# Optimization experiments

Hardware: AMD Instinct MI355X
Metric: run time of the kernel (lower is better)

Reference implementation:

```python
import jax, jax.numpy as jnp
import numpy as np

N_EMBD = 768
N_HEAD = 12


def setup_inputs() -> dict:
    key = jax.random.key(0)
    ks = jax.random.split(key, 5)
    B, T, C = 8, 1024, N_EMBD
    s_in = 1.0 / np.sqrt(C)
    x = jax.random.normal(ks[0], (B, T, C), dtype=jnp.float32)
    w_attn = jax.random.normal(ks[1], (C, 3 * C), dtype=jnp.float32) * s_in
    b_attn = jnp.zeros((3 * C,), dtype=jnp.float32)
    w_proj = jax.random.normal(ks[2], (C, C), dtype=jnp.float32) * s_in
    b_proj = jnp.zeros((C,), dtype=jnp.float32)
    return {"x": x, "w_attn": w_attn, "b_attn": b_attn,
            "w_proj": w_proj, "b_proj": b_proj}


def reference(x, w_attn, b_attn, w_proj, b_proj):
    B, T, C = x.shape
    H, hs = N_HEAD, C // N_HEAD
    qkv = x @ w_attn + b_attn                      # [B,T,3C]
    q, k, v = jnp.split(qkv, 3, axis=-1)
    # [B,H,T,hs]
    q = q.reshape(B, T, H, hs).transpose(0, 2, 1, 3)
    k = k.reshape(B, T, H, hs).transpose(0, 2, 1, 3)
    v = v.reshape(B, T, H, hs).transpose(0, 2, 1, 3)
    att = jnp.einsum('bhqd,bhkd->bhqk', q, k) * (1.0 / np.sqrt(hs))
    causal = jnp.tril(jnp.ones((T, T), dtype=bool))
    att = jnp.where(causal, att, -jnp.inf)
    att = jax.nn.softmax(att, axis=-1)
    y = jnp.einsum('bhqk,bhkd->bhqd', att, v)      # [B,H,T,hs]
    y = y.transpose(0, 2, 1, 3).reshape(B, T, C)
    return y @ w_proj + b_proj
```

## Files before the change

kernel.cpp:

```cpp
#include <hip/hip_runtime.h>
#include <hip/hip_bf16.h>
#include <stdint.h>

typedef unsigned short u16;
typedef short short8 __attribute__((ext_vector_type(8)));
typedef short short4v __attribute__((ext_vector_type(4)));
typedef float floatx4 __attribute__((ext_vector_type(4)));

__device__ __forceinline__ float b2f(u16 v) {
  union { unsigned int u; float f; } c; c.u = ((unsigned int)v) << 16; return c.f;
}
__device__ __forceinline__ u16 f2b(float f) {
  union { float f; unsigned int u; } c; c.f = f;
  unsigned int u = c.u;
  return (u16)((u + 0x7fffu + ((u >> 16) & 1u)) >> 16);
}

__device__ __forceinline__ void gld_lds16(const u16* g, u16* l) {
  __builtin_amdgcn_global_load_lds(
      (const __attribute__((address_space(1))) unsigned int*)g,
      (__attribute__((address_space(3))) unsigned int*)l,
      16, 0, 0);
}

__device__ __forceinline__ void tile_transpose_f2b(
    const float* __restrict__ in, u16* __restrict__ out,
    int inRS, int outRS, int rb, int cb, int tid)
{
  __shared__ __align__(16) u16 t[64][72];
  const int r = tid >> 2, sg = tid & 3;
  const float* ip = in + (long)(rb + r) * inRS + cb + sg * 16;
#pragma unroll
  for (int i = 0; i < 16; i += 4) {
    float4 f = *(const float4*)(ip + i);
    t[r][sg * 16 + i]     = f2b(f.x);
    t[r][sg * 16 + i + 1] = f2b(f.y);
    t[r][sg * 16 + i + 2] = f2b(f.z);
    t[r][sg * 16 + i + 3] = f2b(f.w);
  }
  __syncthreads();
  short8 v0, v1;
#pragma unroll
  for (int i = 0; i < 8; i++) v0[i] = (short)t[sg * 16 + i][r];
#pragma unroll
  for (int i = 0; i < 8; i++) v1[i] = (short)t[sg * 16 + 8 + i][r];
  *(short8*)(out + (long)(cb + r) * outRS + rb + sg * 16)     = v0;
  *(short8*)(out + (long)(cb + r) * outRS + rb + sg * 16 + 8) = v1;
}

__global__ __launch_bounds__(256) void prep(
    const float* __restrict__ x, u16* __restrict__ xb,
    const float* __restrict__ w_attn, u16* __restrict__ wTa,
    const float* __restrict__ w_proj, u16* __restrict__ wTp)
{
  const int bid = blockIdx.x, tid = threadIdx.x;
  if (bid < 6144) {
    int i = (bid * 256 + tid) * 4;
    float4 f = *(const float4*)(x + i);
    short4v v;
    v[0] = (short)f2b(f.x); v[1] = (short)f2b(f.y);
    v[2] = (short)f2b(f.z); v[3] = (short)f2b(f.w);
    *(short4v*)(xb + i) = v;
  } else if (bid < 6576) {
    int t = bid - 6144;
    tile_transpose_f2b(w_attn, wTa, 2304, 768, (t / 36) * 64, (t % 36) * 64, tid);
  } else {
    int t = bid - 6576;
    tile_transpose_f2b(w_proj, wTp, 768, 768, (t / 12) * 64, (t % 12) * 64, tid);
  }
}

__device__ __forceinline__ void store_out(u16* p, float v)  { *p = f2b(v); }
__device__ __forceinline__ void store_out(float* p, float v) { *p = v; }

template <int BM>
__device__ __forceinline__ void stage(
    const u16* __restrict__ A, const u16* __restrict__ Bt,
    long rowbase, long colbase, int K, int k0,
    u16* dA, u16* dB, int tid)
{
  const int c0 = tid, c1 = tid + 256;
  const int ar0 = c0 >> 2, ak0 = (c0 & 3) * 8;
  const int ar1 = c1 >> 2, ak1 = (c1 & 3) * 8;
  gld_lds16(A + (rowbase + ar0) * K + k0 + ak0, dA + c0 * 8);
  if (BM == 128)
    gld_lds16(A + (rowbase + ar1) * K + k0 + ak1, dA + c1 * 8);
  gld_lds16(Bt + (colbase + ar0) * K + k0 + ak0, dB + c0 * 8);
  gld_lds16(Bt + (colbase + ar1) * K + k0 + ak1, dB + c1 * 8);
}

template <typename OT, int BM, bool SPLIT>
__global__ __launch_bounds__(256) void gemm_bt_bias(
    const u16* __restrict__ A, const u16* __restrict__ Bt,
    const float* __restrict__ bias, OT* __restrict__ C, u16* __restrict__ vT,
    int M, int N, int K, int strideC)
{
  constexpr int WNF = (BM == 128) ? 4 : 2;
  __shared__ __align__(16) u16 sA[2][BM * 32];
  __shared__ __align__(16) u16 sB[2][128 * 32];
  const int tid = threadIdx.x;
  const int lane = tid & 63;
  const int wave = tid >> 6;
  const int wm = (BM == 128) ? (wave >> 1) * 64 : 0;
  const int wn = (BM == 128) ? (wave & 1) * 64 : wave * 32;
  const int l15 = lane & 15;
  const int q = lane >> 4;
  const long rowbase = (long)blockIdx.y * BM;
  const long colbase = (long)blockIdx.x * 128;

  floatx4 acc[4][WNF];
#pragma unroll
  for (int i = 0; i < 4; i++)
#pragma unroll
    for (int j = 0; j < WNF; j++) acc[i][j] = (floatx4){0.f, 0.f, 0.f, 0.f};

  stage<BM>(A, Bt, rowbase, colbase, K, 0, sA[0], sB[0], tid);
  __syncthreads();

  const int NIT = K / 32;
  for (int it = 0; it < NIT; ++it) {
    const int cur = it & 1;
    if (it + 1 < NIT)
      stage<BM>(A, Bt, rowbase, colbase, K, (it + 1) * 32, sA[cur ^ 1], sB[cur ^ 1], tid);
    short8 af[4], bf[WNF];
#pragma unroll
    for (int mt = 0; mt < 4; mt++)
      af[mt] = *(const short8*)(sA[cur] + (wm + mt * 16 + l15) * 32 + q * 8);
#pragma unroll
    for (int nt = 0; nt < WNF; nt++)
      bf[nt] = *(const short8*)(sB[cur] + (wn + nt * 16 + l15) * 32 + q * 8);
#pragma unroll
    for (int mt = 0; mt < 4; mt++)
#pragma unroll
      for (int nt = 0; nt < WNF; nt++)
        acc[mt][nt] = __builtin_amdgcn_mfma_f32_16x16x32_bf16(af[mt], bf[nt], acc[mt][nt], 0, 0, 0);
    if (it + 1 < NIT) __syncthreads();
  }

  if (SPLIT && colbase >= 1536) {
    const long b = rowbase >> 10;
    const int t0b = (int)(rowbase & 1023) + wm;
#pragma unroll
    for (int nt = 0; nt < WNF; nt++) {
      const int col = (int)colbase + wn + nt * 16 + l15;
      const float bv = bias[col];
      const int dloc = col - 1536;
      u16* bp = vT + (b * 12 + (dloc >> 6)) * 65536L + (long)(dloc & 63) * 1024;
#pragma unroll
      for (int mt = 0; mt < 4; mt++) {
        short4v pv;
#pragma unroll
        for (int r = 0; r < 4; r++) pv[r] = (short)f2b(acc[mt][nt][r] + bv);
        *(short4v*)(bp + t0b + mt * 16 + q * 4) = pv;
      }
    }
  } else {
#pragma unroll
    for (int nt = 0; nt < WNF; nt++) {
      const long col = colbase + wn + nt * 16 + l15;
      const float bv = bias[col];
#pragma unroll
      for (int mt = 0; mt < 4; mt++)
#pragma unroll
        for (int r = 0; r < 4; r++) {
          const long row = rowbase + wm + mt * 16 + q * 4 + r;
          store_out(C + row * strideC + col, acc[mt][nt][r] + bv);
        }
    }
  }
}

#define QKV_K 768
#define QKV_NT 24

__global__ __launch_bounds__(512, 2) void gemm_qkv_256(
    const u16* __restrict__ A, const u16* __restrict__ Bt,
    const float* __restrict__ bias, u16* __restrict__ qkOut, u16* __restrict__ vT)
{
  __shared__ __align__(16) u16 sA[4][256 * 32];
  __shared__ __align__(16) u16 sB[4][256 * 32];

  const int bid0 = blockIdx.x;
  const int wg = (bid0 & 7) * 36 + (bid0 >> 3);
  const int bx = wg % 9;
  const int by = wg / 9;

  const int tid = threadIdx.x;
  const int lane = tid & 63;
  const int l15 = lane & 15, q = lane >> 4;
  const int wave = tid >> 6;
  const int wm = (wave >> 2) * 128;
  const int wn = (wave & 3) * 64;
  const long rowbase = (long)by * 256;
  const long colbase = (long)bx * 256;
  const int xq = ((q ^ ((l15 >> 1) & 3)) << 3);

  const int ca0 = tid, ca1 = tid + 512;
  const u16* pa0 = A + (rowbase + (ca0 >> 2)) * QKV_K + ((((ca0 & 3) ^ ((ca0 >> 3) & 3))) << 3);
  const u16* pa1 = A + (rowbase + (ca1 >> 2)) * QKV_K + ((((ca1 & 3) ^ ((ca1 >> 3) & 3))) << 3);
  const u16* pb0 = Bt + (colbase + (ca0 >> 2)) * QKV_K + ((((ca0 & 3) ^ ((ca0 >> 3) & 3))) << 3);
  const u16* pb1 = Bt + (colbase + (ca1 >> 2)) * QKV_K + ((((ca1 & 3) ^ ((ca1 >> 3) & 3))) << 3);

#define STAGE_A(t, s) do { \
    gld_lds16(pa0 + (long)(t) * 32, &sA[s][ca0 * 8]); \
    gld_lds16(pa1 + (long)(t) * 32, &sA[s][ca1 * 8]); } while (0)
#define STAGE_B(t, s) do { \
    gld_lds16(pb0 + (long)(t) * 32, &sB[s][ca0 * 8]); \
    gld_lds16(pb1 + (long)(t) * 32, &sB[s][ca1 * 8]); } while (0)

  floatx4 acc[8][4];
#pragma unroll
  for (int i = 0; i < 8; i++)
#pragma unroll
    for (int n = 0; n < 4; n++) acc[i][n] = (floatx4){0.f, 0.f, 0.f, 0.f};

  STAGE_A(0, 0); STAGE_B(0, 0);
  STAGE_A(1, 1); STAGE_B(1, 1);
  STAGE_A(2, 2); STAGE_B(2, 2);
  asm volatile("s_waitcnt vmcnt(8)" ::: "memory");
  __builtin_amdgcn_s_barrier();

#pragma unroll 4
  for (int j = 0; j < QKV_NT; ++j) {
    const int slot = j & 3;
    const u16* ap = sA[slot];
    const u16* bp = sB[slot];

    short8 bf[4];
#pragma unroll
    for (int nt = 0; nt < 4; nt++)
      bf[nt] = *(const short8*)(bp + (wn + nt * 16 + l15) * 32 + xq);
    short8 af[4];
#pragma unroll
    for (int mt = 0; mt < 4; mt++)
      af[mt] = *(const short8*)(ap + (wm + mt * 16 + l15) * 32 + xq);
    if (j + 3 < QKV_NT) STAGE_A(j + 3, (j + 3) & 3);
    __builtin_amdgcn_s_barrier();
    __builtin_amdgcn_s_setprio(1);
#pragma unroll
    for (int mt = 0; mt < 4; mt++)
#pragma unroll
      for (int nt = 0; nt < 4; nt++)
        acc[mt][nt] = __builtin_amdgcn_mfma_f32_16x16x32_bf16(af[mt], bf[nt], acc[mt][nt], 0, 0, 0);
    __builtin_amdgcn_s_setprio(0);

#pragma unroll
    for (int mt = 0; mt < 4; mt++)
      af[mt] = *(const short8*)(ap + (wm + 64 + mt * 16 + l15) * 32 + xq);
    if (j + 3 < QKV_NT) STAGE_B(j + 3, (j + 3) & 3);
    __builtin_amdgcn_s_setprio(1);
#pragma unroll
    for (int mt = 0; mt < 4; mt++)
#pragma unroll
      for (int nt = 0; nt < 4; nt++)
        acc[4 + mt][nt] = __builtin_amdgcn_mfma_f32_16x16x32_bf16(af[mt], bf[nt], acc[4 + mt][nt], 0, 0, 0);
    __builtin_amdgcn_s_setprio(0);

    if (j < QKV_NT - 1) {
      if (j + 3 < QKV_NT)      asm volatile("s_waitcnt vmcnt(8)" ::: "memory");
      else if (j + 2 < QKV_NT) asm volatile("s_waitcnt vmcnt(4)" ::: "memory");
      else                     asm volatile("s_waitcnt vmcnt(0)" ::: "memory");
      __builtin_amdgcn_s_barrier();
    }
  }
#undef STAGE_A
#undef STAGE_B

  if (colbase >= 1536) {
    const long bb = rowbase >> 10;
    const int t0 = (int)(rowbase & 1023) + wm;
#pragma unroll
    for (int nt = 0; nt < 4; nt++) {
      const int col = (int)colbase + wn + nt * 16 + l15;
      const float bv = bias[col];
      const int dloc = col - 1536;
      u16* op = vT + (bb * 12 + (dloc >> 6)) * 65536L + (long)(dloc & 63) * 1024;
#pragma unroll
      for (int mt = 0; mt < 8; mt++) {
        short4v pv;
#pragma unroll
        for (int r = 0; r < 4; r++) pv[r] = (short)f2b(acc[mt][nt][r] + bv);
        *(short4v*)(op + t0 + mt * 16 + q * 4) = pv;
      }
    }
  } else {
#pragma unroll
    for (int nt = 0; nt < 4; nt++) {
      const long col = colbase + wn + nt * 16 + l15;
      const float bv = bias[col];
#pragma unroll
      for (int mt = 0; mt < 8; mt++)
#pragma unroll
        for (int r = 0; r < 4; r++) {
          const long row = rowbase + wm + mt * 16 + q * 4 + r;
          qkOut[row * 1536 + col] = f2b(acc[mt][nt][r] + bv);
        }
    }
  }
}

__global__ __launch_bounds__(256) void attn_fwd(
    const u16* __restrict__ qk, const u16* __restrict__ vT, u16* __restrict__ y)
{
  const int bh = blockIdx.x;
  const int qt = 15 - blockIdx.y;
  const int b = bh / 12, h = bh % 12;
  const long rowOff = (long)b * 1024;
  const int qb = qt * 64;

  __shared__ __align__(16) u16 sK[64 * 72];
  __shared__ __align__(16) u16 sV[2][64 * 72];
  __shared__ __align__(16) u16 sP[64 * 72];

  const int tid = threadIdx.x;
  const int lane = tid & 63, wave = tid >> 6;
  const int l15 = lane & 15, q = lane >> 4;
  const int qrow_g = qb + wave * 16 + l15;

  short8 qf[2];
  {
    const u16* qp = qk + (long)(rowOff + qrow_g) * 1536 + h * 64 + q * 8;
    short8 a0 = *(const short8*)(qp);
    short8 a1 = *(const short8*)(qp + 32);
#pragma unroll
    for (int i = 0; i < 8; i++) {
      a0[i] = (short)f2b(b2f((u16)a0[i]) * 0.125f);
      a1[i] = (short)f2b(b2f((u16)a1[i]) * 0.125f);
    }
    qf[0] = a0; qf[1] = a1;
  }

  float m_i = -1e30f, l_i = 0.f;
  floatx4 o[4];
#pragma unroll
  for (int nt = 0; nt < 4; nt++) o[nt] = (floatx4){0.f, 0.f, 0.f, 0.f};

  for (int j = 0; j <= qt; j++) {
    const int jb = j * 64;
    u16* sVc = sV[j & 1];
#pragma unroll
    for (int rep = 0; rep < 2; rep++) {
      int idx = tid + rep * 256;
      int r = idx >> 3, ch = (idx & 7) * 8;
      *(short8*)(sK + r * 72 + ch) =
          *(const short8*)(qk + (long)(rowOff + jb + r) * 1536 + 768 + h * 64 + ch);
      *(short8*)(sVc + r * 72 + ch) =
          *(const short8*)(vT + (long)bh * 65536 + (long)r * 1024 + jb + ch);
    }
    __syncthreads();

    floatx4 sf[4];
#pragma unroll
    for (int mt = 0; mt < 4; mt++) sf[mt] = (floatx4){0.f, 0.f, 0.f, 0.f};
#pragma unroll
    for (int kk = 0; kk < 2; kk++) {
#pragma unroll
      for (int mt = 0; mt < 4; mt++) {
        short8 kf = *(const short8*)(sK + (mt * 16 + l15) * 72 + kk * 32 + q * 8);
        sf[mt] = __builtin_amdgcn_mfma_f32_16x16x32_bf16(kf, qf[kk], sf[mt], 0, 0, 0);
      }
    }

    float mx = m_i;
#pragma unroll
    for (int mt = 0; mt < 4; mt++)
#pragma unroll
      for (int r = 0; r < 4; r++) {
        int key_g = jb + mt * 16 + q * 4 + r;
        float v = sf[mt][r];
        if (key_g > qrow_g) v = -1e30f;
        sf[mt][r] = v;
        mx = fmaxf(mx, v);
      }
    mx = fmaxf(mx, __shfl_xor(mx, 16));
    mx = fmaxf(mx, __shfl_xor(mx, 32));
    float al = __expf(m_i - mx);
    m_i = mx;
    float rsum = 0.f;
#pragma unroll
    for (int mt = 0; mt < 4; mt++) {
      short4v pv;
#pragma unroll
      for (int r = 0; r < 4; r++) {
        float p = __expf(sf[mt][r] - mx);
        rsum += p;
        pv[r] = (short)f2b(p);
      }
      *(short4v*)(sP + (wave * 16 + l15) * 72 + mt * 16 + q * 4) = pv;
    }
    rsum += __shfl_xor(rsum, 16);
    rsum += __shfl_xor(rsum, 32);
    l_i = l_i * al + rsum;
    __syncthreads();

    float al_r[4];
#pragma unroll
    for (int r = 0; r < 4; r++) al_r[r] = __shfl(al, q * 4 + r);
#pragma unroll
    for (int nt = 0; nt < 4; nt++)
#pragma unroll
      for (int r = 0; r < 4; r++) o[nt][r] *= al_r[r];
#pragma unroll
    for (int kk = 0; kk < 2; kk++) {
      short8 pf = *(const short8*)(sP + (wave * 16 + l15) * 72 + kk * 32 + q * 8);
#pragma unroll
      for (int nt = 0; nt < 4; nt++) {
        short8 vf = *(const short8*)(sVc + (nt * 16 + l15) * 72 + kk * 32 + q * 8);
        o[nt] = __builtin_amdgcn_mfma_f32_16x16x32_bf16(pf, vf, o[nt], 0, 0, 0);
      }
    }
  }

  float linv = 1.f / l_i;
  float li_r[4];
#pragma unroll
  for (int r = 0; r < 4; r++) li_r[r] = __shfl(linv, q * 4 + r);
#pragma unroll
  for (int nt = 0; nt < 4; nt++)
#pragma unroll
    for (int r = 0; r < 4; r++) {
      int row = qb + wave * 16 + q * 4 + r;
      int col = h * 64 + nt * 16 + l15;
      y[(rowOff + row) * 768 + col] = f2b(o[nt][r] * li_r[r]);
    }
}

extern "C" void kernel_launch(void* const* d_in, const int* in_sizes, int n_in,
                              void* d_out, int out_size, void* d_ws, size_t ws_size,
                              hipStream_t stream) {
  const float* x      = (const float*)d_in[0];
  const float* w_attn = (const float*)d_in[1];
  const float* b_attn = (const float*)d_in[2];
  const float* w_proj = (const float*)d_in[3];
  const float* b_proj = (const float*)d_in[4];
  float* out = (float*)d_out;

  char* ws = (char*)d_ws;
  u16* xb   = (u16*)ws; ws += (size_t)8192 * 768 * 2;
  u16* wTa  = (u16*)ws; ws += (size_t)2304 * 768 * 2;
  u16* wTp  = (u16*)ws; ws += (size_t)768 * 768 * 2;
  u16* qk   = (u16*)ws; ws += (size_t)8192 * 1536 * 2;
  u16* vT   = (u16*)ws; ws += (size_t)96 * 64 * 1024 * 2;
  u16* yatt = (u16*)ws; ws += (size_t)8192 * 768 * 2;

  prep<<<dim3(6720), 256, 0, stream>>>(x, xb, w_attn, wTa, w_proj, wTp);

  gemm_qkv_256<<<dim3(288), 512, 0, stream>>>(xb, wTa, b_attn, qk, vT);

  attn_fwd<<<dim3(96, 16), 256, 0, stream>>>(qk, vT, yatt);

  gemm_bt_bias<float, 128, false><<<dim3(6, 64), 256, 0, stream>>>(
      yatt, wTp, b_proj, out, (u16*)nullptr, 8192, 768, 768, 768);
}
```

Measured before the change: 207.9 us.

## Retile QKV GEMM to 256x288 tiles with 12 waves and 256 blocks

Measured after the change: 196.7 us. 5.4% less time.

```diff
diff --git a/kernel.cpp b/kernel.cpp
--- a/kernel.cpp
+++ b/kernel.cpp
@@ -172,52 +172,54 @@
 
 #define QKV_K 768
 #define QKV_NT 24
-
-__global__ __launch_bounds__(512, 2) void gemm_qkv_256(
+#define VMW(n) asm volatile("s_waitcnt vmcnt(" #n ")" ::: "memory")
+
+__global__ __launch_bounds__(768, 3) void gemm_qkv_288(
     const u16* __restrict__ A, const u16* __restrict__ Bt,
     const float* __restrict__ bias, u16* __restrict__ qkOut, u16* __restrict__ vT)
 {
   __shared__ __align__(16) u16 sA[4][256 * 32];
-  __shared__ __align__(16) u16 sB[4][256 * 32];
-
-  const int bid0 = blockIdx.x;
-  const int wg = (bid0 & 7) * 36 + (bid0 >> 3);
-  const int bx = wg % 9;
-  const int by = wg / 9;
+  __shared__ __align__(16) u16 sB[4][288 * 32];
+
+  const int bid = blockIdx.x;
+  const int wg = (bid & 7) * 32 + (bid >> 3);
+  const int bx = wg & 7;
+  const int by = wg >> 3;
 
   const int tid = threadIdx.x;
   const int lane = tid & 63;
   const int l15 = lane & 15, q = lane >> 4;
   const int wave = tid >> 6;
-  const int wm = (wave >> 2) * 128;
-  const int wn = (wave & 3) * 64;
+  const int wm = (wave / 6) * 128;
+  const int wn = (wave % 6) * 48;
   const long rowbase = (long)by * 256;
-  const long colbase = (long)bx * 256;
+  const long colbase = (long)bx * 288;
   const int xq = ((q ^ ((l15 >> 1) & 3)) << 3);
 
-  const int ca0 = tid, ca1 = tid + 512;
-  const u16* pa0 = A + (rowbase + (ca0 >> 2)) * QKV_K + ((((ca0 & 3) ^ ((ca0 >> 3) & 3))) << 3);
-  const u16* pa1 = A + (rowbase + (ca1 >> 2)) * QKV_K + ((((ca1 & 3) ^ ((ca1 >> 3) & 3))) << 3);
-  const u16* pb0 = Bt + (colbase + (ca0 >> 2)) * QKV_K + ((((ca0 & 3) ^ ((ca0 >> 3) & 3))) << 3);
-  const u16* pb1 = Bt + (colbase + (ca1 >> 2)) * QKV_K + ((((ca1 & 3) ^ ((ca1 >> 3) & 3))) << 3);
-
-#define STAGE_A(t, s) do { \
-    gld_lds16(pa0 + (long)(t) * 32, &sA[s][ca0 * 8]); \
-    gld_lds16(pa1 + (long)(t) * 32, &sA[s][ca1 * 8]); } while (0)
-#define STAGE_B(t, s) do { \
-    gld_lds16(pb0 + (long)(t) * 32, &sB[s][ca0 * 8]); \
-    gld_lds16(pb1 + (long)(t) * 32, &sB[s][ca1 * 8]); } while (0)
-
-  floatx4 acc[8][4];
+  const int cA0 = tid, cA1 = 768 + tid;
+  const int cB0 = tid, cB1 = 768 + tid;
+  const u16* pa0 = A + (rowbase + (cA0 >> 2)) * QKV_K + ((((cA0 & 3) ^ ((cA0 >> 3) & 3))) << 3);
+  const u16* pa1 = A + (rowbase + (cA1 >> 2)) * QKV_K + ((((cA1 & 3) ^ ((cA1 >> 3) & 3))) << 3);
+  const u16* pb0 = Bt + (colbase + (cB0 >> 2)) * QKV_K + ((((cB0 & 3) ^ ((cB0 >> 3) & 3))) << 3);
+  const u16* pb1 = Bt + (colbase + (cB1 >> 2)) * QKV_K + ((((cB1 & 3) ^ ((cB1 >> 3) & 3))) << 3);
+  const bool hasA1 = (tid < 256);
+  const bool hasB1 = (tid < 384);
+
+#define STAGE(t, s) do { \
+    const long k0_ = (long)(t) * 32; \
+    gld_lds16(pa0 + k0_, &sA[s][cA0 * 8]); \
+    if (hasA1) gld_lds16(pa1 + k0_, &sA[s][cA1 * 8]); \
+    gld_lds16(pb0 + k0_, &sB[s][cB0 * 8]); \
+    if (hasB1) gld_lds16(pb1 + k0_, &sB[s][cB1 * 8]); } while (0)
+
+  floatx4 acc[8][3];
 #pragma unroll
   for (int i = 0; i < 8; i++)
 #pragma unroll
-    for (int n = 0; n < 4; n++) acc[i][n] = (floatx4){0.f, 0.f, 0.f, 0.f};
-
-  STAGE_A(0, 0); STAGE_B(0, 0);
-  STAGE_A(1, 1); STAGE_B(1, 1);
-  STAGE_A(2, 2); STAGE_B(2, 2);
-  asm volatile("s_waitcnt vmcnt(8)" ::: "memory");
+    for (int n = 0; n < 3; n++) acc[i][n] = (floatx4){0.f, 0.f, 0.f, 0.f};
+
+  STAGE(0, 0); STAGE(1, 1); STAGE(2, 2);
+  if (wave < 4) VMW(8); else if (wave < 6) VMW(6); else VMW(4);
   __builtin_amdgcn_s_barrier();
 
 #pragma unroll 4
@@ -226,55 +228,58 @@
     const u16* ap = sA[slot];
     const u16* bp = sB[slot];
 
-    short8 bf[4];
-#pragma unroll
-    for (int nt = 0; nt < 4; nt++)
+    short8 bf[3];
+#pragma unroll
+    for (int nt = 0; nt < 3; nt++)
       bf[nt] = *(const short8*)(bp + (wn + nt * 16 + l15) * 32 + xq);
     short8 af[4];
 #pragma unroll
     for (int mt = 0; mt < 4; mt++)
       af[mt] = *(const short8*)(ap + (wm + mt * 16 + l15) * 32 + xq);
-    if (j + 3 < QKV_NT) STAGE_A(j + 3, (j + 3) & 3);
+    if (j + 3 < QKV_NT) STAGE(j + 3, (j + 3) & 3);
     __builtin_amdgcn_s_barrier();
     __builtin_amdgcn_s_setprio(1);
 #pragma unroll
     for (int mt = 0; mt < 4; mt++)
 #pragma unroll
-      for (int nt = 0; nt < 4; nt++)
+      for (int nt = 0; nt < 3; nt++)
         acc[mt][nt] = __builtin_amdgcn_mfma_f32_16x16x32_bf16(af[mt], bf[nt], acc[mt][nt], 0, 0, 0);
     __builtin_amdgcn_s_setprio(0);
 
 #pragma unroll
     for (int mt = 0; mt < 4; mt++)
       af[mt] = *(const short8*)(ap + (wm + 64 + mt * 16 + l15) * 32 + xq);
-    if (j + 3 < QKV_NT) STAGE_B(j + 3, (j + 3) & 3);
     __builtin_amdgcn_s_setprio(1);
 #pragma unroll
     for (int mt = 0; mt < 4; mt++)
 #pragma unroll
-      for (int nt = 0; nt < 4; nt++)
+      for (int nt = 0; nt < 3; nt++)
         acc[4 + mt][nt] = __builtin_amdgcn_mfma_f32_16x16x32_bf16(af[mt], bf[nt], acc[4 + mt][nt], 0, 0, 0);
     __builtin_amdgcn_s_setprio(0);
 
     if (j < QKV_NT - 1) {
-      if (j + 3 < QKV_NT)      asm volatile("s_waitcnt vmcnt(8)" ::: "memory");
-      else if (j + 2 < QKV_NT) asm volatile("s_waitcnt vmcnt(4)" ::: "memory");
-      else                     asm volatile("s_waitcnt vmcnt(0)" ::: "memory");
+      if (j + 3 < QKV_NT) {
+        if (wave < 4) VMW(8); else if (wave < 6) VMW(6); else VMW(4);
+      } else if (j + 2 < QKV_NT) {
+        if (wave < 4) VMW(4); else if (wave < 6) VMW(3); else VMW(2);
+      } else {
+        VMW(0);
+      }
       __builtin_amdgcn_s_barrier();
     }
   }
-#undef STAGE_A
-#undef STAGE_B
-
-  if (colbase >= 1536) {
-    const long bb = rowbase >> 10;
-    const int t0 = (int)(rowbase & 1023) + wm;
-#pragma unroll
-    for (int nt = 0; nt < 4; nt++) {
-      const int col = (int)colbase + wn + nt * 16 + l15;
-      const float bv = bias[col];
+#undef STAGE
+
+#pragma unroll
+  for (int nt = 0; nt < 3; nt++) {
+    const int fragc = (int)colbase + wn + nt * 16;
+    const int col = fragc + l15;
+    const float bv = bias[col];
+    if (fragc >= 1536) {
+      const long bb = rowbase >> 10;
       const int dloc = col - 1536;
       u16* op = vT + (bb * 12 + (dloc >> 6)) * 65536L + (long)(dloc & 63) * 1024;
+      const int t0 = (int)(rowbase & 1023) + wm;
 #pragma unroll
       for (int mt = 0; mt < 8; mt++) {
         short4v pv;
@@ -282,12 +287,7 @@
         for (int r = 0; r < 4; r++) pv[r] = (short)f2b(acc[mt][nt][r] + bv);
         *(short4v*)(op + t0 + mt * 16 + q * 4) = pv;
       }
-    }
-  } else {
-#pragma unroll
-    for (int nt = 0; nt < 4; nt++) {
-      const long col = colbase + wn + nt * 16 + l15;
-      const float bv = bias[col];
+    } else {
 #pragma unroll
       for (int mt = 0; mt < 8; mt++)
 #pragma unroll
@@ -298,6 +298,7 @@
     }
   }
 }
+#undef VMW
 
 __global__ __launch_bounds__(256) void attn_fwd(
     const u16* __restrict__ qk, const u16* __restrict__ vT, u16* __restrict__ y)
@@ -445,7 +446,7 @@
 
   prep<<<dim3(6720), 256, 0, stream>>>(x, xb, w_attn, wTa, w_proj, wTp);
 
-  gemm_qkv_256<<<dim3(288), 512, 0, stream>>>(xb, wTa, b_attn, qk, vT);
+  gemm_qkv_288<<<dim3(256), 768, 0, stream>>>(xb, wTa, b_attn, qk, vT);
 
   attn_fwd<<<dim3(96, 16), 256, 0, stream>>>(qk, vT, yatt);
 
```
